# Optimization experiments

Measured on AMD Instinct MI355X. Metric: run time of the kernel, lower is better.

The kernel has to match this reference:

```python
import jax, jax.numpy as jnp
import numpy as np

N = 100000      # nodes
E = 1600000     # edges (avg degree 16)
G = 2000        # graphs
D_IN = 4        # node_in_dim
H = 128         # hidden_dim
L = 3           # num_layers


def setup_inputs() -> dict:
    key = jax.random.key(0)
    ks = jax.random.split(key, 16)
    si = 1.0 / np.sqrt(D_IN)
    sh = 1.0 / np.sqrt(H)
    inp = {
        "x": jax.random.normal(ks[0], (N, D_IN), jnp.float32),
        "edge_index": jax.random.randint(ks[1], (2, E), 0, N, dtype=jnp.int32),
        "batch": jnp.sort(jax.random.randint(ks[2], (N,), 0, G, dtype=jnp.int32)),
        "proj_w": jax.random.normal(ks[3], (D_IN, H), jnp.float32) * si,
        "proj_b": jnp.zeros((H,), jnp.float32),
        "conv_w1": jax.random.normal(ks[4], (L, H, H), jnp.float32) * sh,
        "conv_b1": jnp.zeros((L, H), jnp.float32),
        "conv_w2": jax.random.normal(ks[5], (L, H, H), jnp.float32) * sh,
        "conv_b2": jnp.zeros((L, H), jnp.float32),
        "shared_w": jax.random.normal(ks[6], (H, H), jnp.float32) * sh,
        "shared_b": jnp.zeros((H,), jnp.float32),
        "e_w": jax.random.normal(ks[7], (H, 1), jnp.float32) * sh,
        "e_b": jnp.zeros((1,), jnp.float32),
        "d_w": jax.random.normal(ks[8], (H, 1), jnp.float32) * sh,
        "d_b": jnp.zeros((1,), jnp.float32),
    }
    return inp


def reference(x, edge_index, batch, proj_w, proj_b, conv_w1, conv_b1,
              conv_w2, conv_b2, shared_w, shared_b, e_w, e_b, d_w, d_b):
    src, dst = edge_index[0], edge_index[1]
    # input projection: [N, D_IN] -> [N, H]
    h = x @ proj_w + proj_b
    # GIN layers: h' = relu(MLP((1+eps)*h + sum_{j->i} h_j)), eps = 0
    for l in range(L):
        agg = jax.ops.segment_sum(h[src], dst, num_segments=N)  # scatter-add
        m = h + agg
        m = jax.nn.relu(m @ conv_w1[l] + conv_b1[l]) @ conv_w2[l] + conv_b2[l]
        h = jax.nn.relu(m)
    # global mean pool over graphs: [N, H] -> [G, H]
    sums = jax.ops.segment_sum(h, batch, num_segments=G)
    cnt = jax.ops.segment_sum(jnp.ones((N,), h.dtype), batch, num_segments=G)
    g = sums / jnp.maximum(cnt, 1.0)[:, None]
    # shared head (dropout inactive in eval)
    g = jax.nn.relu(g @ shared_w + shared_b)
    energy = (g @ e_w + e_b).reshape(-1)
    dipole = (g @ d_w + d_b).reshape(-1)
    return (energy, dipole)
```

## Files before the change

### kernel.cpp

```cpp
#include <hip/hip_runtime.h>
#include <hip/hip_bf16.h>

#define H 128
#define REGSZ 512
#define PCHUNK 4096

typedef short short8 __attribute__((ext_vector_type(8)));
typedef float f32x4 __attribute__((ext_vector_type(4)));

__device__ __forceinline__ float bf2f(unsigned short u) {
    union { unsigned int i; float f; } c; c.i = ((unsigned int)u) << 16; return c.f;
}
__device__ __forceinline__ unsigned short f2bf(float f) {
    return __builtin_bit_cast(unsigned short, __float2bfloat16(f));
}
__device__ __forceinline__ uint2 pack_fp8x8(const float* f) {
    unsigned int lo = 0, hi = 0;
    lo = __builtin_amdgcn_cvt_pk_fp8_f32(f[0], f[1], lo, 0);
    lo = __builtin_amdgcn_cvt_pk_fp8_f32(f[2], f[3], lo, 1);
    hi = __builtin_amdgcn_cvt_pk_fp8_f32(f[4], f[5], hi, 0);
    hi = __builtin_amdgcn_cvt_pk_fp8_f32(f[6], f[7], hi, 1);
    return make_uint2(lo, hi);
}
__device__ __forceinline__ void unpack_fp8x8(uint2 v, float* f) {
    f[0] = __builtin_amdgcn_cvt_f32_fp8(v.x, 0);
    f[1] = __builtin_amdgcn_cvt_f32_fp8(v.x, 1);
    f[2] = __builtin_amdgcn_cvt_f32_fp8(v.x, 2);
    f[3] = __builtin_amdgcn_cvt_f32_fp8(v.x, 3);
    f[4] = __builtin_amdgcn_cvt_f32_fp8(v.y, 0);
    f[5] = __builtin_amdgcn_cvt_f32_fp8(v.y, 1);
    f[6] = __builtin_amdgcn_cvt_f32_fp8(v.y, 2);
    f[7] = __builtin_amdgcn_cvt_f32_fp8(v.y, 3);
}

__global__ void prep_w_kernel(const float* __restrict__ cw1, const float* __restrict__ cw2,
                              unsigned short* __restrict__ wt, int total) {
    int idx = blockIdx.x * 256 + threadIdx.x;
    if (idx >= total) return;
    int m = idx >> 14;
    int o = (idx >> 7) & 127;
    int i = idx & 127;
    const float* srcp = (m < 3) ? (cw1 + (size_t)m * H * H) : (cw2 + (size_t)(m - 3) * H * H);
    wt[idx] = f2bf(srcp[i * H + o]);
}

__global__ void proj_kernel(const float* __restrict__ x, const float* __restrict__ pw,
                            const float* __restrict__ pb, unsigned char* __restrict__ h8, int N) {
    int tid = blockIdx.x * 256 + threadIdx.x;
    if (tid >= N * 16) return;
    int i = tid >> 4, c = (tid & 15) * 8;
    float4 xv = *(const float4*)&x[i * 4];
    float acc[8];
#pragma unroll
    for (int j = 0; j < 8; ++j)
        acc[j] = pb[c + j] + xv.x * pw[0 * H + c + j] + xv.y * pw[1 * H + c + j]
               + xv.z * pw[2 * H + c + j] + xv.w * pw[3 * H + c + j];
    *(uint2*)&h8[(size_t)i * H + c] = pack_fp8x8(acc);
}

__global__ __launch_bounds__(256) void partition_kernel(
    const int* __restrict__ src, const int* __restrict__ dst,
    int* __restrict__ rcnt, int* __restrict__ bucket,
    int E, int nreg, int cap) {
    __shared__ int hcnt[256];
    __shared__ int hbase[256];
    int tid = threadIdx.x;
    hcnt[tid] = 0;
    __syncthreads();
    int e0 = blockIdx.x * PCHUNK;
    int e1 = min(e0 + PCHUNK, E);
    for (int e = e0 + tid; e < e1; e += 256)
        atomicAdd(&hcnt[dst[e] >> 9], 1);
    __syncthreads();
    {
        int c = hcnt[tid];
        hbase[tid] = (c > 0) ? atomicAdd(&rcnt[tid], c) : 0;
        hcnt[tid] = 0;
    }
    __syncthreads();
    for (int e = e0 + tid; e < e1; e += 256) {
        int d = dst[e], s = src[e];
        int r = d >> 9;
        int pos = hbase[r] + atomicAdd(&hcnt[r], 1);
        if (pos < cap) bucket[(size_t)r * cap + pos] = ((d & (REGSZ - 1)) << 17) | s;
    }
}

__global__ __launch_bounds__(256) void csr_region_kernel(
    const int* __restrict__ rcnt, const int* __restrict__ bucket,
    int* __restrict__ offs, int* __restrict__ esrc,
    int N, int nreg, int cap) {
    __shared__ int cnt[REGSZ];
    __shared__ int part[256];
    __shared__ int sbase;
    int r = blockIdx.x;
    int tid = threadIdx.x;

    int v = (tid < nreg) ? rcnt[tid] : 0;
    part[tid] = v;
    __syncthreads();
    for (int off = 1; off < 256; off <<= 1) {
        int t = (tid >= off) ? part[tid - off] : 0;
        __syncthreads();
        part[tid] += t;
        __syncthreads();
    }
    if (tid == 0) sbase = (r == 0) ? 0 : part[r - 1];
    cnt[tid] = 0;
    cnt[tid + 256] = 0;
    __syncthreads();
    int base = sbase;
    int n = min(part[r] - base, cap);
    const int* bk = bucket + (size_t)r * cap;

    for (int p = tid; p < n; p += 256)
        atomicAdd(&cnt[bk[p] >> 17], 1);
    __syncthreads();

    int c0 = cnt[tid * 2], c1 = cnt[tid * 2 + 1];
    part[tid] = c0 + c1;
    __syncthreads();
    for (int off = 1; off < 256; off <<= 1) {
        int t = (tid >= off) ? part[tid - off] : 0;
        __syncthreads();
        part[tid] += t;
        __syncthreads();
    }
    int excl = (tid == 0) ? 0 : part[tid - 1];
    cnt[tid * 2] = excl;
    cnt[tid * 2 + 1] = excl + c0;
    __syncthreads();

    for (int p = tid; p < n; p += 256) {
        int e = bk[p];
        int pos = atomicAdd(&cnt[e >> 17], 1);
        esrc[base + pos] = e & 0x1FFFF;
    }
    __syncthreads();

    int lo = r * REGSZ;
#pragma unroll
    for (int i = tid; i < REGSZ; i += 256) {
        int node = lo + i;
        if (node < N) offs[node] = base + cnt[i];
    }
}

__global__ void gather_agg_kernel(const int* __restrict__ offs, const int* __restrict__ esrc,
                                  const unsigned char* __restrict__ h8, unsigned short* __restrict__ pre, int N) {
    int tid = blockIdx.x * 256 + threadIdx.x;
    if (tid >= N * 16) return;
    int node = tid >> 4, c = (tid & 15) * 8;
    int s = (node == 0) ? 0 : offs[node - 1];
    int e = offs[node];
    float acc[8];
    unpack_fp8x8(*(const uint2*)&h8[(size_t)node * H + c], acc);
    int i = s;
    for (; i + 3 < e; i += 4) {
        uint2 v[4];
#pragma unroll
        for (int k = 0; k < 4; ++k) v[k] = *(const uint2*)&h8[(size_t)esrc[i + k] * H + c];
#pragma unroll
        for (int k = 0; k < 4; ++k) {
            acc[0] += __builtin_amdgcn_cvt_f32_fp8(v[k].x, 0);
            acc[1] += __builtin_amdgcn_cvt_f32_fp8(v[k].x, 1);
            acc[2] += __builtin_amdgcn_cvt_f32_fp8(v[k].x, 2);
            acc[3] += __builtin_amdgcn_cvt_f32_fp8(v[k].x, 3);
            acc[4] += __builtin_amdgcn_cvt_f32_fp8(v[k].y, 0);
            acc[5] += __builtin_amdgcn_cvt_f32_fp8(v[k].y, 1);
            acc[6] += __builtin_amdgcn_cvt_f32_fp8(v[k].y, 2);
            acc[7] += __builtin_amdgcn_cvt_f32_fp8(v[k].y, 3);
        }
    }
    for (; i < e; ++i) {
        uint2 v = *(const uint2*)&h8[(size_t)esrc[i] * H + c];
        acc[0] += __builtin_amdgcn_cvt_f32_fp8(v.x, 0);
        acc[1] += __builtin_amdgcn_cvt_f32_fp8(v.x, 1);
        acc[2] += __builtin_amdgcn_cvt_f32_fp8(v.x, 2);
        acc[3] += __builtin_amdgcn_cvt_f32_fp8(v.x, 3);
        acc[4] += __builtin_amdgcn_cvt_f32_fp8(v.y, 0);
        acc[5] += __builtin_amdgcn_cvt_f32_fp8(v.y, 1);
        acc[6] += __builtin_amdgcn_cvt_f32_fp8(v.y, 2);
        acc[7] += __builtin_amdgcn_cvt_f32_fp8(v.y, 3);
    }
    short8 o;
#pragma unroll
    for (int j = 0; j < 8; ++j) o[j] = (short)f2bf(acc[j]);
    *(short8*)&pre[(size_t)node * H + c] = o;
}

template <bool LAST>
__global__ __launch_bounds__(512) void fused_mlp_kernel(
    const unsigned short* __restrict__ pre,
    const unsigned short* __restrict__ W1t, const unsigned short* __restrict__ W2t,
    const float* __restrict__ b1, const float* __restrict__ b2,
    unsigned char* __restrict__ h8, const int* __restrict__ batch,
    float* __restrict__ gsum, int N) {
    __shared__ unsigned short As[128 * H];
    __shared__ unsigned short Ws1[H * H];
    __shared__ unsigned short Ws2[H * H];
    __shared__ int sbatch[128];
    int bm = blockIdx.x * 128;
    int tid = threadIdx.x;

#pragma unroll
    for (int rep = 0; rep < 4; ++rep) {
        int lin = rep * 512 + tid;
        int r = lin >> 4, cb = lin & 15;
        int row = bm + r;
        short8 vv = {};
        if (row < N) vv = *(const short8*)&pre[(size_t)row * H + cb * 8];
        int byte = r * 256 + ((cb * 16) ^ ((r & 7) << 4));
        *(short8*)((char*)As + byte) = vv;
    }
#pragma unroll
    for (int rep = 0; rep < 4; ++rep) {
        int lin = rep * 512 + tid;
        int o = lin >> 4, cb = lin & 15;
        int byte = o * 256 + ((cb * 16) ^ ((o & 7) << 4));
        *(short8*)((char*)Ws1 + byte) = *(const short8*)&W1t[(size_t)o * H + cb * 8];
        *(short8*)((char*)Ws2 + byte) = *(const short8*)&W2t[(size_t)o * H + cb * 8];
    }
    if (LAST && tid < 128) {
        int row = bm + tid;
        sbatch[tid] = (row < N) ? batch[row] : -1;
    }
    __syncthreads();

    int lane = tid & 63;
    int w = tid >> 6;
    int wr = (w >> 1) * 32;
    int wc = (w & 1) * 64;
    int lrow = lane & 15, kg = lane >> 4;

    float b1v[4], b2v[4];
#pragma unroll
    for (int ct = 0; ct < 4; ++ct) {
        b1v[ct] = b1[wc + ct * 16 + lrow];
        b2v[ct] = b2[wc + ct * 16 + lrow];
    }

    short8 a[2][4];
#pragma unroll
    for (int rt = 0; rt < 2; ++rt)
#pragma unroll
        for (int ks = 0; ks < 4; ++ks) {
            int r = wr + rt * 16 + lrow;
            int kb = ks * 64 + kg * 16;
            a[rt][ks] = *(short8*)((char*)As + r * 256 + (kb ^ ((r & 7) << 4)));
        }

    f32x4 acc[2][4] = {};
#pragma unroll
    for (int ct = 0; ct < 4; ++ct) {
#pragma unroll
        for (int ks = 0; ks < 4; ++ks) {
            int o = wc + ct * 16 + lrow;
            int kb = ks * 64 + kg * 16;
            short8 b = *(short8*)((char*)Ws1 + o * 256 + (kb ^ ((o & 7) << 4)));
            acc[0][ct] = __builtin_amdgcn_mfma_f32_16x16x32_bf16(a[0][ks], b, acc[0][ct], 0, 0, 0);
            acc[1][ct] = __builtin_amdgcn_mfma_f32_16x16x32_bf16(a[1][ks], b, acc[1][ct], 0, 0, 0);
        }
    }
    __syncthreads();

#pragma unroll
    for (int rt = 0; rt < 2; ++rt)
#pragma unroll
        for (int ct = 0; ct < 4; ++ct)
#pragma unroll
            for (int rr = 0; rr < 4; ++rr) {
                int r = wr + rt * 16 + kg * 4 + rr;
                int col = wc + ct * 16 + lrow;
                float v = fmaxf(acc[rt][ct][rr] + b1v[ct], 0.f);
                int byte = r * 256 + ((col * 2) ^ ((r & 7) << 4));
                *(unsigned short*)((char*)As + byte) = f2bf(v);
            }
    __syncthreads();

#pragma unroll
    for (int rt = 0; rt < 2; ++rt)
#pragma unroll
        for (int ks = 0; ks < 4; ++ks) {
            int r = wr + rt * 16 + lrow;
            int kb = ks * 64 + kg * 16;
            a[rt][ks] = *(short8*)((char*)As + r * 256 + (kb ^ ((r & 7) << 4)));
        }

    f32x4 acc2[2][4] = {};
#pragma unroll
    for (int ct = 0; ct < 4; ++ct) {
#pragma unroll
        for (int ks = 0; ks < 4; ++ks) {
            int o = wc + ct * 16 + lrow;
            int kb = ks * 64 + kg * 16;
            short8 b = *(short8*)((char*)Ws2 + o * 256 + (kb ^ ((o & 7) << 4)));
            acc2[0][ct] = __builtin_amdgcn_mfma_f32_16x16x32_bf16(a[0][ks], b, acc2[0][ct], 0, 0, 0);
            acc2[1][ct] = __builtin_amdgcn_mfma_f32_16x16x32_bf16(a[1][ks], b, acc2[1][ct], 0, 0, 0);
        }
    }
    __syncthreads();

#pragma unroll
    for (int rt = 0; rt < 2; ++rt)
#pragma unroll
        for (int ct = 0; ct < 4; ++ct)
#pragma unroll
            for (int rr = 0; rr < 4; ++rr) {
                int r = wr + rt * 16 + kg * 4 + rr;
                int col = wc + ct * 16 + lrow;
                float v = fmaxf(acc2[rt][ct][rr] + b2v[ct], 0.f);
                As[r * H + col] = f2bf(v);
            }
    __syncthreads();

    if (!LAST) {
#pragma unroll
        for (int rep = 0; rep < 4; ++rep) {
            int lin = rep * 512 + tid;
            int r = lin >> 4, cb = lin & 15;
            int row = bm + r;
            if (row < N) {
                short8 v = *(short8*)&As[r * H + cb * 8];
                float f[8];
#pragma unroll
                for (int j = 0; j < 8; ++j) f[j] = bf2f((unsigned short)v[j]);
                *(uint2*)&h8[(size_t)row * H + cb * 8] = pack_fp8x8(f);
            }
        }
    } else {
        int col = tid & 127;
        int rg = tid >> 7;
        int r0 = rg * 32;
        int rmax = min(r0 + 32, N - bm);
        if (r0 < rmax) {
            float accp = 0.f;
            int cur = sbatch[r0];
            for (int r = r0; r < rmax; ++r) {
                int g = sbatch[r];
                if (g != cur) {
                    atomicAdd(&gsum[(size_t)cur * H + col], accp);
                    cur = g;
                    accp = 0.f;
                }
                accp += bf2f(As[r * H + col]);
            }
            atomicAdd(&gsum[(size_t)cur * H + col], accp);
        }
    }
}

__global__ __launch_bounds__(128) void head_kernel(
    const float* __restrict__ gsum, const int* __restrict__ batch,
    const float* __restrict__ sw, const float* __restrict__ sb,
    const float* __restrict__ ew, const float* __restrict__ eb,
    const float* __restrict__ dw, const float* __restrict__ db,
    float* __restrict__ out, int N, int G) {
    int g = blockIdx.x;
    int j = threadIdx.x;
    int s, e;
    {
        int lo = 0, hi = N;
        while (lo < hi) { int mid = (lo + hi) >> 1; if (batch[mid] < g) lo = mid + 1; else hi = mid; }
        s = lo;
        hi = N;
        while (lo < hi) { int mid = (lo + hi) >> 1; if (batch[mid] < g + 1) lo = mid + 1; else hi = mid; }
        e = lo;
    }
    float cnt = (float)(e - s);
    __shared__ float gm[H];
    gm[j] = gsum[(size_t)g * H + j] / fmaxf(cnt, 1.0f);
    __syncthreads();
    float t = sb[j];
    for (int k = 0; k < H; ++k) t += gm[k] * sw[k * H + j];
    t = fmaxf(t, 0.f);
    __shared__ float red[2][H];
    red[0][j] = t * ew[j];
    red[1][j] = t * dw[j];
    __syncthreads();
    for (int off = 64; off > 0; off >>= 1) {
        if (j < off) {
            red[0][j] += red[0][j + off];
            red[1][j] += red[1][j + off];
        }
        __syncthreads();
    }
    if (j == 0) {
        out[g] = red[0][0] + eb[0];
        out[G + g] = red[1][0] + db[0];
    }
}

extern "C" void kernel_launch(void* const* d_in, const int* in_sizes, int n_in,
                              void* d_out, int out_size, void* d_ws, size_t ws_size,
                              hipStream_t stream) {
    const float* x      = (const float*)d_in[0];
    const int*   ei     = (const int*)d_in[1];
    const int*   batch  = (const int*)d_in[2];
    const float* proj_w = (const float*)d_in[3];
    const float* proj_b = (const float*)d_in[4];
    const float* cw1    = (const float*)d_in[5];
    const float* cb1    = (const float*)d_in[6];
    const float* cw2    = (const float*)d_in[7];
    const float* cb2    = (const float*)d_in[8];
    const float* sw     = (const float*)d_in[9];
    const float* sb     = (const float*)d_in[10];
    const float* ew     = (const float*)d_in[11];
    const float* eb     = (const float*)d_in[12];
    const float* dw     = (const float*)d_in[13];
    const float* db     = (const float*)d_in[14];

    int N = in_sizes[0] / 4;
    int E = in_sizes[1] / 2;
    int G = out_size / 2;

    const int* src = ei;
    const int* dst = ei + E;

    unsigned short* pre = (unsigned short*)d_ws;
    unsigned short* wt  = pre + (size_t)N * H;
    int* offs  = (int*)(wt + 6 * H * H);
    int* rcnt  = offs + N + 1;
    float* gsum = (float*)(rcnt + 256);
    int* esrc  = (int*)(gsum + (size_t)G * H);
    unsigned char* h8 = (unsigned char*)(esrc + E);
    int* bucket = (int*)pre;

    float* out = (float*)d_out;

    int nreg = (N + REGSZ - 1) >> 9;
    int cap  = (E / nreg) * 5 / 4 + 1024;

    hipMemsetAsync(rcnt, 0, (256 + (size_t)G * H) * sizeof(int), stream);

    partition_kernel<<<(E + PCHUNK - 1) / PCHUNK, 256, 0, stream>>>(src, dst, rcnt, bucket, E, nreg, cap);
    csr_region_kernel<<<nreg, 256, 0, stream>>>(rcnt, bucket, offs, esrc, N, nreg, cap);

    prep_w_kernel<<<(6 * H * H + 255) / 256, 256, 0, stream>>>(cw1, cw2, wt, 6 * H * H);
    proj_kernel<<<(N * 16 + 255) / 256, 256, 0, stream>>>(x, proj_w, proj_b, h8, N);

    int mlp_blocks = (N + 127) / 128;
    int gather_blocks = (N * 16 + 255) / 256;

    for (int l = 0; l < 3; ++l) {
        gather_agg_kernel<<<gather_blocks, 256, 0, stream>>>(offs, esrc, h8, pre, N);
        if (l < 2)
            fused_mlp_kernel<false><<<mlp_blocks, 512, 0, stream>>>(
                pre, wt + (size_t)l * H * H, wt + (size_t)(3 + l) * H * H,
                cb1 + l * H, cb2 + l * H, h8, batch, gsum, N);
        else
            fused_mlp_kernel<true><<<mlp_blocks, 512, 0, stream>>>(
                pre, wt + (size_t)l * H * H, wt + (size_t)(3 + l) * H * H,
                cb1 + l * H, cb2 + l * H, h8, batch, gsum, N);
    }

    head_kernel<<<G, 128, 0, stream>>>(gsum, batch, sw, sb, ew, eb, dw, db, out, N, G);
}
```

Baseline: 319.5 us.

## Store node features in column-group-major slices for cache-local gathers

Node features (fp8 h and bf16 pre-activation) move from row-major [N,128] to eight column-group slices of [N,16]. Each gather block handles one 16-column slice for 256 nodes, and each thread owns one node, loading 16 bytes per neighbour. The aim is to shrink the working set per slice (1.6 MB) so random neighbour reads stay in cache, and to cut redundant index and offset loads. In exchange, every gather thread must walk its node's whole edge list, and the MLP load and store paths now use strided slice accesses.

```diff
diff --git a/kernel.cpp b/kernel.cpp
--- a/kernel.cpp
+++ b/kernel.cpp
@@ -22,15 +22,11 @@
     hi = __builtin_amdgcn_cvt_pk_fp8_f32(f[6], f[7], hi, 1);
     return make_uint2(lo, hi);
 }
-__device__ __forceinline__ void unpack_fp8x8(uint2 v, float* f) {
-    f[0] = __builtin_amdgcn_cvt_f32_fp8(v.x, 0);
-    f[1] = __builtin_amdgcn_cvt_f32_fp8(v.x, 1);
-    f[2] = __builtin_amdgcn_cvt_f32_fp8(v.x, 2);
-    f[3] = __builtin_amdgcn_cvt_f32_fp8(v.x, 3);
-    f[4] = __builtin_amdgcn_cvt_f32_fp8(v.y, 0);
-    f[5] = __builtin_amdgcn_cvt_f32_fp8(v.y, 1);
-    f[6] = __builtin_amdgcn_cvt_f32_fp8(v.y, 2);
-    f[7] = __builtin_amdgcn_cvt_f32_fp8(v.y, 3);
+__device__ __forceinline__ void unpack_word(unsigned int w, float* f) {
+    f[0] = __builtin_amdgcn_cvt_f32_fp8(w, 0);
+    f[1] = __builtin_amdgcn_cvt_f32_fp8(w, 1);
+    f[2] = __builtin_amdgcn_cvt_f32_fp8(w, 2);
+    f[3] = __builtin_amdgcn_cvt_f32_fp8(w, 3);
 }
 
 __global__ void prep_w_kernel(const float* __restrict__ cw1, const float* __restrict__ cw2,
@@ -45,17 +41,23 @@
 }
 
 __global__ void proj_kernel(const float* __restrict__ x, const float* __restrict__ pw,
-                            const float* __restrict__ pb, unsigned char* __restrict__ h8, int N) {
-    int tid = blockIdx.x * 256 + threadIdx.x;
-    if (tid >= N * 16) return;
-    int i = tid >> 4, c = (tid & 15) * 8;
-    float4 xv = *(const float4*)&x[i * 4];
-    float acc[8];
-#pragma unroll
-    for (int j = 0; j < 8; ++j)
-        acc[j] = pb[c + j] + xv.x * pw[0 * H + c + j] + xv.y * pw[1 * H + c + j]
-               + xv.z * pw[2 * H + c + j] + xv.w * pw[3 * H + c + j];
-    *(uint2*)&h8[(size_t)i * H + c] = pack_fp8x8(acc);
+                            const float* __restrict__ pb, unsigned char* __restrict__ h8t, int N) {
+    int bid = blockIdx.x;
+    int cg = bid & 7;
+    int node = (bid >> 3) * 256 + threadIdx.x;
+    if (node >= N) return;
+    float4 xv = *(const float4*)&x[node * 4];
+    int c0 = cg * 16;
+    float acc[16];
+#pragma unroll
+    for (int j = 0; j < 16; ++j) {
+        int col = c0 + j;
+        acc[j] = pb[col] + xv.x * pw[0 * H + col] + xv.y * pw[1 * H + col]
+               + xv.z * pw[2 * H + col] + xv.w * pw[3 * H + col];
+    }
+    uint2 p0 = pack_fp8x8(acc);
+    uint2 p1 = pack_fp8x8(acc + 8);
+    *(uint4*)&h8t[((size_t)cg * N + node) * 16] = make_uint4(p0.x, p0.y, p1.x, p1.y);
 }
 
 __global__ __launch_bounds__(256) void partition_kernel(
@@ -147,54 +149,65 @@
 }
 
 __global__ void gather_agg_kernel(const int* __restrict__ offs, const int* __restrict__ esrc,
-                                  const unsigned char* __restrict__ h8, unsigned short* __restrict__ pre, int N) {
-    int tid = blockIdx.x * 256 + threadIdx.x;
-    if (tid >= N * 16) return;
-    int node = tid >> 4, c = (tid & 15) * 8;
+                                  const unsigned char* __restrict__ h8t, unsigned short* __restrict__ pre_t, int N) {
+    int bid = blockIdx.x;
+    int cg = bid & 7;
+    int node = (bid >> 3) * 256 + threadIdx.x;
+    if (node >= N) return;
+    const unsigned char* slice = h8t + (size_t)cg * N * 16;
     int s = (node == 0) ? 0 : offs[node - 1];
     int e = offs[node];
-    float acc[8];
-    unpack_fp8x8(*(const uint2*)&h8[(size_t)node * H + c], acc);
+    float acc[16];
+    {
+        uint4 sv = *(const uint4*)&slice[(size_t)node * 16];
+        unpack_word(sv.x, acc);
+        unpack_word(sv.y, acc + 4);
+        unpack_word(sv.z, acc + 8);
+        unpack_word(sv.w, acc + 12);
+    }
     int i = s;
     for (; i + 3 < e; i += 4) {
-        uint2 v[4];
-#pragma unroll
-        for (int k = 0; k < 4; ++k) v[k] = *(const uint2*)&h8[(size_t)esrc[i + k] * H + c];
+        uint4 v[4];
+#pragma unroll
+        for (int k = 0; k < 4; ++k) v[k] = *(const uint4*)&slice[(size_t)esrc[i + k] * 16];
 #pragma unroll
         for (int k = 0; k < 4; ++k) {
-            acc[0] += __builtin_amdgcn_cvt_f32_fp8(v[k].x, 0);
-            acc[1] += __builtin_amdgcn_cvt_f32_fp8(v[k].x, 1);
-            acc[2] += __builtin_amdgcn_cvt_f32_fp8(v[k].x, 2);
-            acc[3] += __builtin_amdgcn_cvt_f32_fp8(v[k].x, 3);
-            acc[4] += __builtin_amdgcn_cvt_f32_fp8(v[k].y, 0);
-            acc[5] += __builtin_amdgcn_cvt_f32_fp8(v[k].y, 1);
-            acc[6] += __builtin_amdgcn_cvt_f32_fp8(v[k].y, 2);
-            acc[7] += __builtin_amdgcn_cvt_f32_fp8(v[k].y, 3);
+            float t[16];
+            unpack_word(v[k].x, t);
+            unpack_word(v[k].y, t + 4);
+            unpack_word(v[k].z, t + 8);
+            unpack_word(v[k].w, t + 12);
+#pragma unroll
+            for (int j = 0; j < 16; ++j) acc[j] += t[j];
         }
     }
     for (; i < e; ++i) {
-        uint2 v = *(const uint2*)&h8[(size_t)esrc[i] * H + c];
-        acc[0] += __builtin_amdgcn_cvt_f32_fp8(v.x, 0);
-        acc[1] += __builtin_amdgcn_cvt_f32_fp8(v.x, 1);
-        acc[2] += __builtin_amdgcn_cvt_f32_fp8(v.x, 2);
-        acc[3] += __builtin_amdgcn_cvt_f32_fp8(v.x, 3);
-        acc[4] += __builtin_amdgcn_cvt_f32_fp8(v.y, 0);
-        acc[5] += __builtin_amdgcn_cvt_f32_fp8(v.y, 1);
-        acc[6] += __builtin_amdgcn_cvt_f32_fp8(v.y, 2);
-        acc[7] += __builtin_amdgcn_cvt_f32_fp8(v.y, 3);
-    }
-    short8 o;
-#pragma unroll
-    for (int j = 0; j < 8; ++j) o[j] = (short)f2bf(acc[j]);
-    *(short8*)&pre[(size_t)node * H + c] = o;
+        uint4 v = *(const uint4*)&slice[(size_t)esrc[i] * 16];
+        float t[16];
+        unpack_word(v.x, t);
+        unpack_word(v.y, t + 4);
+        unpack_word(v.z, t + 8);
+        unpack_word(v.w, t + 12);
+#pragma unroll
+        for (int j = 0; j < 16; ++j) acc[j] += t[j];
+    }
+    short8 o0, o1;
+#pragma unroll
+    for (int j = 0; j < 8; ++j) {
+        o0[j] = (short)f2bf(acc[j]);
+        o1[j] = (short)f2bf(acc[8 + j]);
+    }
+    unsigned short* dst = pre_t + ((size_t)cg * N + node) * 16;
+    *(short8*)dst = o0;
+    *(short8*)(dst + 8) = o1;
 }
 
 template <bool LAST>
 __global__ __launch_bounds__(512) void fused_mlp_kernel(
-    const unsigned short* __restrict__ pre,
+    const unsigned short* __restrict__ pre_t,
     const unsigned short* __restrict__ W1t, const unsigned short* __restrict__ W2t,
     const float* __restrict__ b1, const float* __restrict__ b2,
-    unsigned char* __restrict__ h8, const int* __restrict__ batch,
+    unsigned char* __restrict__ h8t, const int* __restrict__ batch,
     float* __restrict__ gsum, int N) {
     __shared__ unsigned short As[128 * H];
     __shared__ unsigned short Ws1[H * H];
@@ -204,14 +217,19 @@
     int tid = threadIdx.x;
 
 #pragma unroll
-    for (int rep = 0; rep < 4; ++rep) {
+    for (int rep = 0; rep < 2; ++rep) {
         int lin = rep * 512 + tid;
-        int r = lin >> 4, cb = lin & 15;
+        int r = lin & 127, cg = lin >> 7;
         int row = bm + r;
-        short8 vv = {};
-        if (row < N) vv = *(const short8*)&pre[(size_t)row * H + cb * 8];
-        int byte = r * 256 + ((cb * 16) ^ ((r & 7) << 4));
-        *(short8*)((char*)As + byte) = vv;
+        short8 v0 = {}, v1 = {};
+        if (row < N) {
+            const unsigned short* p = pre_t + ((size_t)cg * N + row) * 16;
+            v0 = *(const short8*)p;
+            v1 = *(const short8*)(p + 8);
+        }
+        int sw = (r & 7) << 4;
+        *(short8*)((char*)As + r * 256 + ((cg * 32) ^ sw)) = v0;
+        *(short8*)((char*)As + r * 256 + ((cg * 32 + 16) ^ sw)) = v1;
     }
 #pragma unroll
     for (int rep = 0; rep < 4; ++rep) {
@@ -316,16 +334,17 @@
 
     if (!LAST) {
 #pragma unroll
-        for (int rep = 0; rep < 4; ++rep) {
+        for (int rep = 0; rep < 2; ++rep) {
             int lin = rep * 512 + tid;
-            int r = lin >> 4, cb = lin & 15;
+            int r = lin & 127, cg = lin >> 7;
             int row = bm + r;
             if (row < N) {
-                short8 v = *(short8*)&As[r * H + cb * 8];
-                float f[8];
-#pragma unroll
-                for (int j = 0; j < 8; ++j) f[j] = bf2f((unsigned short)v[j]);
-                *(uint2*)&h8[(size_t)row * H + cb * 8] = pack_fp8x8(f);
+                float f[16];
+#pragma unroll
+                for (int j = 0; j < 16; ++j) f[j] = bf2f(As[r * H + cg * 16 + j]);
+                uint2 p0 = pack_fp8x8(f);
+                uint2 p1 = pack_fp8x8(f + 8);
+                *(uint4*)&h8t[((size_t)cg * N + row) * 16] = make_uint4(p0.x, p0.y, p1.x, p1.y);
             }
         }
     } else {
@@ -436,14 +455,14 @@
     partition_kernel<<<(E + PCHUNK - 1) / PCHUNK, 256, 0, stream>>>(src, dst, rcnt, bucket, E, nreg, cap);
     csr_region_kernel<<<nreg, 256, 0, stream>>>(rcnt, bucket, offs, esrc, N, nreg, cap);
 
+    int nchunk = (N + 255) / 256;
     prep_w_kernel<<<(6 * H * H + 255) / 256, 256, 0, stream>>>(cw1, cw2, wt, 6 * H * H);
-    proj_kernel<<<(N * 16 + 255) / 256, 256, 0, stream>>>(x, proj_w, proj_b, h8, N);
+    proj_kernel<<<nchunk * 8, 256, 0, stream>>>(x, proj_w, proj_b, h8, N);
 
     int mlp_blocks = (N + 127) / 128;
-    int gather_blocks = (N * 16 + 255) / 256;
 
     for (int l = 0; l < 3; ++l) {
-        gather_agg_kernel<<<gather_blocks, 256, 0, stream>>>(offs, esrc, h8, pre, N);
+        gather_agg_kernel<<<nchunk * 8, 256, 0, stream>>>(offs, esrc, h8, pre, N);
         if (l < 2)
             fused_mlp_kernel<false><<<mlp_blocks, 512, 0, stream>>>(
                 pre, wt + (size_t)l * H * H, wt + (size_t)(3 + l) * H * H,
```

After: 389.7 us. 1.22x slower.
